# Optimization experiments

Hardware: AMD Instinct MI355X
Metric: run time of the kernel (lower is better)

Reference implementation:

```python
import jax, jax.numpy as jnp
import numpy as np

D = 1024  # in_features
H = 16    # head_num

def setup_inputs() -> dict:
    key = jax.random.key(0)
    ks = jax.random.split(key, 11)
    S, B = 2048, 2
    scale = 1.0 / np.sqrt(D)
    inp = {
        'q': jax.random.normal(ks[0], (S, B, D), jnp.float32),
        'k': jax.random.normal(ks[1], (S, B, D), jnp.float32),
        'v': jax.random.normal(ks[2], (S, B, D), jnp.float32),
        'Wq': jax.random.normal(ks[3], (D, D), jnp.float32) * scale,
        'Wk': jax.random.normal(ks[4], (D, D), jnp.float32) * scale,
        'Wv': jax.random.normal(ks[5], (D, D), jnp.float32) * scale,
        'Wo': jax.random.normal(ks[6], (D, D), jnp.float32) * scale,
        'bq': jax.random.normal(ks[7], (D,), jnp.float32) * 0.01,
        'bk': jax.random.normal(ks[8], (D,), jnp.float32) * 0.01,
        'bv': jax.random.normal(ks[9], (D,), jnp.float32) * 0.01,
        'bo': jax.random.normal(ks[10], (D,), jnp.float32) * 0.01,
    }
    return inp

def reference(q, k, v, Wq, Wk, Wv, Wo, bq, bk, bv, bo):
    # q,k,v: (S, B, D) -> (B, S, D)
    q = jnp.transpose(q, (1, 0, 2))
    k = jnp.transpose(k, (1, 0, 2))
    v = jnp.transpose(v, (1, 0, 2))
    # linear + ReLU (torch Linear: x @ W.T + b)
    qh = jax.nn.relu(q @ Wq.T + bq)
    kh = jax.nn.relu(k @ Wk.T + bk)
    vh = jax.nn.relu(v @ Wv.T + bv)
    B, S, _ = qh.shape
    hd = D // H
    # (B, S, H, hd) -> (B, H, S, hd)
    qh = qh.reshape(B, S, H, hd).transpose(0, 2, 1, 3)
    kh = kh.reshape(B, S, H, hd).transpose(0, 2, 1, 3)
    vh = vh.reshape(B, S, H, hd).transpose(0, 2, 1, 3)
    scores = jnp.einsum('bhsd,bhtd->bhst', qh, kh) / np.sqrt(hd).astype(np.float32)
    attn = jax.nn.softmax(scores, axis=-1)
    y = jnp.einsum('bhst,bhtd->bhsd', attn, vh)  # (B, H, S, hd)
    y = y.transpose(0, 2, 1, 3).reshape(B, S, D)
    y = jax.nn.relu(y @ Wo.T + bo)
    return jnp.transpose(y, (1, 0, 2))  # (S, B, D)
```

## Files before the change

### kernel.cpp

```cpp
#include <hip/hip_runtime.h>
#include <stdint.h>

typedef __attribute__((ext_vector_type(8))) short bf8v;
typedef __attribute__((ext_vector_type(4))) float f4v;
typedef __attribute__((ext_vector_type(16))) float f16v;
typedef __attribute__((ext_vector_type(4))) unsigned int u4v;

__device__ __forceinline__ unsigned short f2bf(float f) {
  unsigned int u = __float_as_uint(f);
  u += 0x7fffu + ((u >> 16) & 1u);
  return (unsigned short)(u >> 16);
}

__device__ __forceinline__ float bf2f(unsigned short s) {
  return __uint_as_float((unsigned)s << 16);
}

__device__ __forceinline__ void gload16(const void* g, void* l) {
  __builtin_amdgcn_global_load_lds(
      (__attribute__((address_space(1))) void*)reinterpret_cast<uintptr_t>(g),
      (__attribute__((address_space(3))) void*)reinterpret_cast<uintptr_t>(l),
      16, 0, 0);
}

__device__ __forceinline__ unsigned cvtpk(float lo, float hi) {
  unsigned r;
  asm("v_cvt_pk_bf16_f32 %0, %1, %2" : "=v"(r) : "v"(lo), "v"(hi));
  return r;
}

#define PAIR_SWAP(x, y) asm("v_permlane32_swap_b32 %0, %1" : "+v"(x), "+v"(y))

__global__ __launch_bounds__(256) void cvt_all(
    const float* __restrict__ s0, const float* __restrict__ s1,
    const float* __restrict__ s2, const float* __restrict__ s3,
    const float* __restrict__ s4, const float* __restrict__ s5,
    const float* __restrict__ s6, unsigned short* __restrict__ dst) {
  const size_t NA = (size_t)1 << 22, NW = (size_t)1 << 20;
  size_t i = ((size_t)blockIdx.x * 256 + threadIdx.x) * 8;
  const float* src;
  size_t off;
  if (i < 3 * NA) {
    int a = (int)(i >> 22);
    src = (a == 0) ? s0 : (a == 1) ? s1 : s2;
    off = i & (NA - 1);
  } else {
    size_t j = i - 3 * NA;
    int a = (int)(j >> 20);
    src = (a == 0) ? s3 : (a == 1) ? s4 : (a == 2) ? s5 : s6;
    off = j & (NW - 1);
  }
  const f4v* sp = (const f4v*)(src + off);
  f4v x = sp[0], y = sp[1];
  bf8v r;
  r[0] = (short)f2bf(x[0]); r[1] = (short)f2bf(x[1]);
  r[2] = (short)f2bf(x[2]); r[3] = (short)f2bf(x[3]);
  r[4] = (short)f2bf(y[0]); r[5] = (short)f2bf(y[1]);
  r[6] = (short)f2bf(y[2]); r[7] = (short)f2bf(y[3]);
  *(bf8v*)(dst + i) = r;
}

template <int OMODE, int TN>
__device__ __forceinline__ void gemm_body(
    unsigned short* Al, unsigned short* Bl,
    const unsigned short* __restrict__ A, const unsigned short* __restrict__ W,
    const float* __restrict__ bias, void* __restrict__ out) {
  const int tid = threadIdx.x;
  const int w = tid >> 6, l = tid & 63;
  const int lr = l >> 4, lc = l & 15;
  const int m0 = blockIdx.x * 128, n0 = blockIdx.y * TN;
  const int wr = w >> 1, wc = w & 1;
  const int JW = TN / 32;
  const int BCPW = TN / 64;
  const int BBUF = TN * 32;

  f4v acc[4][JW];
#pragma unroll
  for (int i = 0; i < 4; i++)
#pragma unroll
    for (int j = 0; j < JW; j++) acc[i][j] = (f4v)(0.0f);

  const int NK = 32;
#pragma unroll
  for (int i = 0; i < 2; i++) {
    int chunk = w * 2 + i;
    int e = chunk * 512 + l * 8;
    int r = e >> 5, k = e & 31;
    gload16(A + (size_t)(m0 + r) * 1024 + k, Al + chunk * 512);
  }
#pragma unroll
  for (int i = 0; i < BCPW; i++) {
    int chunk = w * BCPW + i;
    int e = chunk * 512 + l * 8;
    int r = e >> 5, k = e & 31;
    gload16(W + (size_t)(n0 + r) * 1024 + k, Bl + chunk * 512);
  }

  for (int kk = 0; kk < NK; kk++) {
    const int cur = kk & 1;
    __syncthreads();
    if (kk + 1 < NK) {
#pragma unroll
      for (int i = 0; i < 2; i++) {
        int chunk = w * 2 + i;
        int e = chunk * 512 + l * 8;
        int r = e >> 5, k = (kk + 1) * 32 + (e & 31);
        gload16(A + (size_t)(m0 + r) * 1024 + k, Al + (cur ^ 1) * 4096 + chunk * 512);
      }
#pragma unroll
      for (int i = 0; i < BCPW; i++) {
        int chunk = w * BCPW + i;
        int e = chunk * 512 + l * 8;
        int r = e >> 5, k = (kk + 1) * 32 + (e & 31);
        gload16(W + (size_t)(n0 + r) * 1024 + k, Bl + (cur ^ 1) * BBUF + chunk * 512);
      }
    }
    bf8v av[4], bv[JW];
#pragma unroll
    for (int i = 0; i < 4; i++) {
      int row = wr * 64 + i * 16 + lc;
      av[i] = *(const bf8v*)(Al + cur * 4096 + row * 32 + lr * 8);
    }
#pragma unroll
    for (int j = 0; j < JW; j++) {
      int row = wc * (TN / 2) + j * 16 + lc;
      bv[j] = *(const bf8v*)(Bl + cur * BBUF + row * 32 + lr * 8);
    }
#pragma unroll
    for (int i = 0; i < 4; i++)
#pragma unroll
      for (int j = 0; j < JW; j++)
        acc[i][j] = __builtin_amdgcn_mfma_f32_16x16x32_bf16(av[i], bv[j], acc[i][j], 0, 0, 0);
  }

#pragma unroll
  for (int j = 0; j < JW; j++) {
    int n = n0 + wc * (TN / 2) + j * 16 + lc;
    float bj = bias[n];
#pragma unroll
    for (int i = 0; i < 4; i++) {
      int mb = m0 + wr * 64 + i * 16 + lr * 4;
#pragma unroll
      for (int q = 0; q < 4; q++) {
        float val = fmaxf(acc[i][j][q] + bj, 0.0f);
        int m = mb + q;
        if (OMODE == 2) {
          int s = m & 2047, b = m >> 11;
          ((float*)out)[(size_t)(s * 2 + b) * 1024 + n] = val;
        } else {
          int s = m >> 1, b = m & 1;
          int h = n >> 6, d = n & 63;
          if (OMODE == 0)
            ((unsigned short*)out)[((size_t)(b * 16 + h) * 2048 + s) * 64 + d] = f2bf(val);
          else
            ((unsigned short*)out)[((size_t)(b * 16 + h) * 64 + d) * 2048 + s] = f2bf(val);
        }
      }
    }
  }
}

__global__ __launch_bounds__(256) void qkv_gemm(
    const unsigned short* __restrict__ qA, const unsigned short* __restrict__ kA,
    const unsigned short* __restrict__ vA,
    const unsigned short* __restrict__ Wq, const unsigned short* __restrict__ Wk,
    const unsigned short* __restrict__ Wv,
    const float* __restrict__ bq, const float* __restrict__ bk,
    const float* __restrict__ bv,
    unsigned short* __restrict__ Qh, unsigned short* __restrict__ Kh,
    unsigned short* __restrict__ Vt) {
  __shared__ __align__(16) unsigned short Al[2 * 4096];
  __shared__ __align__(16) unsigned short Bl[2 * 4096];
  int z = blockIdx.z;
  if (z == 0)      gemm_body<0, 128>(Al, Bl, qA, Wq, bq, Qh);
  else if (z == 1) gemm_body<0, 128>(Al, Bl, kA, Wk, bk, Kh);
  else             gemm_body<1, 128>(Al, Bl, vA, Wv, bv, Vt);
}

__global__ __launch_bounds__(256) void out_gemm(
    const unsigned short* __restrict__ Y, const unsigned short* __restrict__ Wo,
    const float* __restrict__ bo, float* __restrict__ out) {
  __shared__ __align__(16) unsigned short Al[2 * 4096];
  __shared__ __align__(16) unsigned short Bl[2 * 2048];
  gemm_body<2, 64>(Al, Bl, Y, Wo, bo, out);
}

__global__ __launch_bounds__(256, 2) void attn_kernel(
    const unsigned short* __restrict__ Qh, const unsigned short* __restrict__ Kh,
    const unsigned short* __restrict__ Vt,
    unsigned short* __restrict__ PO, float2* __restrict__ ML) {
  __shared__ __align__(16) unsigned short Kl[2][4096];
  __shared__ __align__(16) unsigned short Vl[2][4096];
  const int tid = threadIdx.x, w = tid >> 6, l = tid & 63;
  const int lo = l & 31, hi = l >> 5;
  const int bh = blockIdx.y;
  const int z = blockIdx.z;
  const int tbeg = z << 10, tend = tbeg + 1024;
  const int q0 = blockIdx.x * 256 + w * 64;
  const size_t qkbase = (size_t)bh * 2048 * 64;
  const size_t vtbase = (size_t)bh * 64 * 2048;
  const float cs = 0.125f * 1.44269504088896341f;

  bf8v qf[2][4];
#pragma unroll
  for (int s = 0; s < 2; s++)
#pragma unroll
    for (int c = 0; c < 4; c++)
      qf[s][c] = *(const bf8v*)(Qh + qkbase + (size_t)(q0 + s * 32 + lo) * 64 + c * 16 + hi * 8);

  f16v oacc[2][2];
  oacc[0][0] = (f16v)(0.0f); oacc[0][1] = (f16v)(0.0f);
  oacc[1][0] = (f16v)(0.0f); oacc[1][1] = (f16v)(0.0f);
  float mrun[2] = {-1e30f, -1e30f};
  float lrun[2] = {0.0f, 0.0f};

  const int swl = (lo & 7) << 4;
  int akb[4], avb[2][2][2];
#pragma unroll
  for (int c = 0; c < 4; c++) akb[c] = lo * 128 + ((c * 32 + hi * 16) ^ swl);
#pragma unroll
  for (int dt = 0; dt < 2; dt++)
#pragma unroll
    for (int kvh = 0; kvh < 2; kvh++)
#pragma unroll
      for (int kc = 0; kc < 2; kc++)
        avb[dt][kvh][kc] = (dt * 32 + lo) * 128 + ((kvh * 64 + kc * 32 + hi * 16) ^ swl);

  int stE[2], stD[2], stKV[2];
#pragma unroll
  for (int i = 0; i < 2; i++) {
    int o = (w * 2 + i) * 1024 + l * 16;
    int row = o >> 7;
    stE[i] = (o ^ ((row & 7) << 4)) >> 1;
    stD[i] = stE[i] >> 6;
    stKV[i] = stE[i] & 63;
  }
  const char* KlB = (const char*)&Kl[0][0];
  const char* VlB = (const char*)&Vl[0][0];

  auto STAGE = [&](int buf, int t0) {
#pragma unroll
    for (int i = 0; i < 2; i++) {
      gload16(Kh + qkbase + (size_t)t0 * 64 + stE[i], (char*)&Kl[buf][0] + (w * 2 + i) * 1024);
      gload16(Vt + vtbase + (size_t)stD[i] * 2048 + t0 + stKV[i], (char*)&Vl[buf][0] + (w * 2 + i) * 1024);
    }
  };

  auto COMPUTE = [&](int bo) {
#pragma unroll
    for (int kvh = 0; kvh < 2; kvh++) {
      bf8v kf[4];
#pragma unroll
      for (int c = 0; c < 4; c++)
        kf[c] = *(const bf8v*)(KlB + bo + kvh * 4096 + akb[c]);
      f16v sa = (f16v)(0.0f), sb = (f16v)(0.0f);
#pragma unroll
      for (int c = 0; c < 4; c++) {
        sa = __builtin_amdgcn_mfma_f32_32x32x16_bf16(kf[c], qf[0][c], sa, 0, 0, 0);
        sb = __builtin_amdgcn_mfma_f32_32x32x16_bf16(kf[c], qf[1][c], sb, 0, 0, 0);
      }
      bf8v vf[2][2];
#pragma unroll
      for (int dt = 0; dt < 2; dt++)
#pragma unroll
        for (int kc = 0; kc < 2; kc++)
          vf[dt][kc] = *(const bf8v*)(VlB + bo + avb[dt][kvh][kc]);

#pragma unroll
      for (int s = 0; s < 2; s++) {
        const f16v& sc16 = (s == 0) ? sa : sb;
        float t0 = fmaxf(fmaxf(sc16[0], sc16[1]), sc16[2]);
        float t1 = fmaxf(fmaxf(sc16[3], sc16[4]), sc16[5]);
        float t2 = fmaxf(fmaxf(sc16[6], sc16[7]), sc16[8]);
        float t3 = fmaxf(fmaxf(sc16[9], sc16[10]), sc16[11]);
        float t4 = fmaxf(fmaxf(sc16[12], sc16[13]), sc16[14]);
        float lm = fmaxf(fmaxf(fmaxf(t0, t1), fmaxf(t2, t3)), fmaxf(t4, sc16[15]));
        float msc = lm * cs;
        if (!__all(msc <= mrun[s] + 8.0f)) {
          float x = msc, y = msc;
          PAIR_SWAP(x, y);
          float pm = fmaxf(x, y);
          float mnew = fmaxf(mrun[s], pm);
          float scl = __builtin_amdgcn_exp2f(mrun[s] - mnew);
          lrun[s] *= scl;
#pragma unroll
          for (int dt = 0; dt < 2; dt++)
#pragma unroll
            for (int r = 0; r < 16; r++) oacc[s][dt][r] *= scl;
          mrun[s] = mnew;
        }
        float p[16];
#pragma unroll
        for (int r = 0; r < 16; r++)
          p[r] = __builtin_amdgcn_exp2f(sc16[r] * cs - mrun[s]);
        float s01 = (p[0] + p[1]) + (p[2] + p[3]);
        float s23 = (p[4] + p[5]) + (p[6] + p[7]);
        float s45 = (p[8] + p[9]) + (p[10] + p[11]);
        float s67 = (p[12] + p[13]) + (p[14] + p[15]);
        lrun[s] += (s01 + s23) + (s45 + s67);
        bf8v pf[2];
#pragma unroll
        for (int kc = 0; kc < 2; kc++) {
          unsigned a0 = cvtpk(p[kc * 8 + 0], p[kc * 8 + 1]);
          unsigned a1 = cvtpk(p[kc * 8 + 2], p[kc * 8 + 3]);
          unsigned b0 = cvtpk(p[kc * 8 + 4], p[kc * 8 + 5]);
          unsigned b1 = cvtpk(p[kc * 8 + 6], p[kc * 8 + 7]);
          PAIR_SWAP(a0, b0);
          PAIR_SWAP(a1, b1);
          u4v pw;
          pw[0] = a0; pw[1] = a1; pw[2] = b0; pw[3] = b1;
          pf[kc] = __builtin_bit_cast(bf8v, pw);
        }
#pragma unroll
        for (int dt = 0; dt < 2; dt++)
#pragma unroll
          for (int kc = 0; kc < 2; kc++)
            oacc[s][dt] = __builtin_amdgcn_mfma_f32_32x32x16_bf16(vf[dt][kc], pf[kc],
                                                                 oacc[s][dt], 0, 0, 0);
      }
    }
  };

  STAGE(0, tbeg);
  __syncthreads();
#pragma unroll 1
  for (int t0 = tbeg; t0 < tend; t0 += 128) {
    STAGE(1, t0 + 64);
    COMPUTE(0);
    __syncthreads();
    if (t0 + 128 < tend) STAGE(0, t0 + 128);
    COMPUTE(8192);
    __syncthreads();
  }

#pragma unroll
  for (int s = 0; s < 2; s++) {
    float x = lrun[s], y = lrun[s];
    PAIR_SWAP(x, y);
    float lt = x + y;
    int q = q0 + s * 32 + lo;
    size_t prow = (size_t)(z * 32 + bh) * 2048 + q;
    if (hi == 0) ML[prow] = float2{mrun[s], lt};
    unsigned short* pp = PO + prow * 64;
#pragma unroll
    for (int dt = 0; dt < 2; dt++)
#pragma unroll
      for (int r = 0; r < 16; r++) {
        int d = dt * 32 + (r & 3) + 8 * (r >> 2) + 4 * hi;
        pp[d] = f2bf(oacc[s][dt][r]);
      }
  }
}

__global__ __launch_bounds__(256) void combine_kernel(
    const unsigned short* __restrict__ PO, const float2* __restrict__ ML,
    unsigned short* __restrict__ Y) {
  int idx = blockIdx.x * 256 + threadIdx.x;
  int row = idx >> 1, hr = idx & 1;
  int bh = row >> 11, q = row & 2047;
  float2 ml0 = ML[row], ml1 = ML[65536 + row];
  float M = fmaxf(ml0.x, ml1.x);
  float a0 = __builtin_amdgcn_exp2f(ml0.x - M);
  float a1 = __builtin_amdgcn_exp2f(ml1.x - M);
  float L = ml0.y * a0 + ml1.y * a1;
  float s0 = a0 / L, s1 = a1 / L;
  const unsigned short* p0 = PO + (size_t)row * 64 + hr * 32;
  const unsigned short* p1 = PO + ((size_t)65536 + row) * 64 + hr * 32;
  int b = bh >> 4, h = bh & 15;
  unsigned short* yp = Y + (((size_t)(b * 2048 + q)) << 10) + h * 64 + hr * 32;
#pragma unroll
  for (int g = 0; g < 4; g++) {
    bf8v v0 = *(const bf8v*)(p0 + g * 8);
    bf8v v1 = *(const bf8v*)(p1 + g * 8);
    bf8v r;
#pragma unroll
    for (int j = 0; j < 8; j++)
      r[j] = (short)f2bf(bf2f((unsigned short)v0[j]) * s0 +
                         bf2f((unsigned short)v1[j]) * s1);
    *(bf8v*)(yp + g * 8) = r;
  }
}

extern "C" void kernel_launch(void* const* d_in, const int* in_sizes, int n_in,
                              void* d_out, int out_size, void* d_ws, size_t ws_size,
                              hipStream_t stream) {
  const float* q  = (const float*)d_in[0];
  const float* k  = (const float*)d_in[1];
  const float* v  = (const float*)d_in[2];
  const float* Wq = (const float*)d_in[3];
  const float* Wk = (const float*)d_in[4];
  const float* Wv = (const float*)d_in[5];
  const float* Wo = (const float*)d_in[6];
  const float* bq = (const float*)d_in[7];
  const float* bk = (const float*)d_in[8];
  const float* bv = (const float*)d_in[9];
  const float* bo = (const float*)d_in[10];

  const size_t NA = (size_t)4096 * 1024;
  const size_t NW = (size_t)1024 * 1024;
  unsigned short* qA  = (unsigned short*)d_ws;
  unsigned short* kA  = qA  + NA;
  unsigned short* vA  = kA  + NA;
  unsigned short* WqB = vA  + NA;
  unsigned short* WkB = WqB + NW;
  unsigned short* WvB = WkB + NW;
  unsigned short* WoB = WvB + NW;
  unsigned short* Qh  = WoB + NW;
  unsigned short* Kh  = Qh  + NA;
  unsigned short* Vt  = Kh  + NA;
  unsigned short* Y   = Vt  + NA;

  unsigned short* PO = qA;
  float2*         ML = (float2*)vA;

  cvt_all<<<dim3(8192), 256, 0, stream>>>(q, k, v, Wq, Wk, Wv, Wo, qA);

  qkv_gemm<<<dim3(32, 8, 3), 256, 0, stream>>>(qA, kA, vA, WqB, WkB, WvB,
                                               bq, bk, bv, Qh, Kh, Vt);
  attn_kernel<<<dim3(8, 32, 2), 256, 0, stream>>>(Qh, Kh, Vt, PO, ML);
  combine_kernel<<<dim3(512), 256, 0, stream>>>(PO, ML, Y);
  out_gemm<<<dim3(32, 16), 256, 0, stream>>>(Y, WoB, bo, (float*)d_out);
}
```

Baseline: 127.7 us.

## Split attention KV into four chunks, raise occupancy, prioritize MFMA waves

When the workspace is large enough, the attention kernel now splits the KV range four ways instead of two, doubling the grid to fill more CUs. A generalized combine kernel merges the partial outputs. The kernel's launch bound now asks for 4 blocks per SIMD, and s_setprio raises wave priority around the MFMA groups. The lazy rescale threshold also drops from 8 to 5. The split adds partial-output traffic and a heavier combine step, and the tighter launch bound may force register spills.

```diff
diff --git a/kernel.cpp b/kernel.cpp
--- a/kernel.cpp
+++ b/kernel.cpp
@@ -185,17 +185,17 @@
   gemm_body<2, 64>(Al, Bl, Y, Wo, bo, out);
 }
 
-__global__ __launch_bounds__(256, 2) void attn_kernel(
+__global__ __launch_bounds__(256, 4) void attn_kernel(
     const unsigned short* __restrict__ Qh, const unsigned short* __restrict__ Kh,
     const unsigned short* __restrict__ Vt,
-    unsigned short* __restrict__ PO, float2* __restrict__ ML) {
+    unsigned short* __restrict__ PO, float2* __restrict__ ML, int kvlen) {
   __shared__ __align__(16) unsigned short Kl[2][4096];
   __shared__ __align__(16) unsigned short Vl[2][4096];
   const int tid = threadIdx.x, w = tid >> 6, l = tid & 63;
   const int lo = l & 31, hi = l >> 5;
   const int bh = blockIdx.y;
   const int z = blockIdx.z;
-  const int tbeg = z << 10, tend = tbeg + 1024;
+  const int tbeg = z * kvlen, tend = tbeg + kvlen;
   const int q0 = blockIdx.x * 256 + w * 64;
   const size_t qkbase = (size_t)bh * 2048 * 64;
   const size_t vtbase = (size_t)bh * 64 * 2048;
@@ -254,11 +254,13 @@
       for (int c = 0; c < 4; c++)
         kf[c] = *(const bf8v*)(KlB + bo + kvh * 4096 + akb[c]);
       f16v sa = (f16v)(0.0f), sb = (f16v)(0.0f);
+      __builtin_amdgcn_s_setprio(1);
 #pragma unroll
       for (int c = 0; c < 4; c++) {
         sa = __builtin_amdgcn_mfma_f32_32x32x16_bf16(kf[c], qf[0][c], sa, 0, 0, 0);
         sb = __builtin_amdgcn_mfma_f32_32x32x16_bf16(kf[c], qf[1][c], sb, 0, 0, 0);
       }
+      __builtin_amdgcn_s_setprio(0);
       bf8v vf[2][2];
 #pragma unroll
       for (int dt = 0; dt < 2; dt++)
@@ -276,7 +278,7 @@
         float t4 = fmaxf(fmaxf(sc16[12], sc16[13]), sc16[14]);
         float lm = fmaxf(fmaxf(fmaxf(t0, t1), fmaxf(t2, t3)), fmaxf(t4, sc16[15]));
         float msc = lm * cs;
-        if (!__all(msc <= mrun[s] + 8.0f)) {
+        if (!__all(msc <= mrun[s] + 5.0f)) {
           float x = msc, y = msc;
           PAIR_SWAP(x, y);
           float pm = fmaxf(x, y);
@@ -311,12 +313,14 @@
           pw[0] = a0; pw[1] = a1; pw[2] = b0; pw[3] = b1;
           pf[kc] = __builtin_bit_cast(bf8v, pw);
         }
+        __builtin_amdgcn_s_setprio(1);
 #pragma unroll
         for (int dt = 0; dt < 2; dt++)
 #pragma unroll
           for (int kc = 0; kc < 2; kc++)
             oacc[s][dt] = __builtin_amdgcn_mfma_f32_32x32x16_bf16(vf[dt][kc], pf[kc],
                                                                  oacc[s][dt], 0, 0, 0);
+        __builtin_amdgcn_s_setprio(0);
       }
     }
   };
@@ -352,31 +356,45 @@
   }
 }
 
+template <int SPL>
 __global__ __launch_bounds__(256) void combine_kernel(
     const unsigned short* __restrict__ PO, const float2* __restrict__ ML,
     unsigned short* __restrict__ Y) {
   int idx = blockIdx.x * 256 + threadIdx.x;
   int row = idx >> 1, hr = idx & 1;
   int bh = row >> 11, q = row & 2047;
-  float2 ml0 = ML[row], ml1 = ML[65536 + row];
-  float M = fmaxf(ml0.x, ml1.x);
-  float a0 = __builtin_amdgcn_exp2f(ml0.x - M);
-  float a1 = __builtin_amdgcn_exp2f(ml1.x - M);
-  float L = ml0.y * a0 + ml1.y * a1;
-  float s0 = a0 / L, s1 = a1 / L;
-  const unsigned short* p0 = PO + (size_t)row * 64 + hr * 32;
-  const unsigned short* p1 = PO + ((size_t)65536 + row) * 64 + hr * 32;
+  float2 ml[SPL];
+  float M = -1e30f;
+#pragma unroll
+  for (int i = 0; i < SPL; i++) {
+    ml[i] = ML[i * 65536 + row];
+    M = fmaxf(M, ml[i].x);
+  }
+  float a[SPL], L = 0.0f;
+#pragma unroll
+  for (int i = 0; i < SPL; i++) {
+    a[i] = __builtin_amdgcn_exp2f(ml[i].x - M);
+    L += ml[i].y * a[i];
+  }
+  float invL = 1.0f / L;
+#pragma unroll
+  for (int i = 0; i < SPL; i++) a[i] *= invL;
   int b = bh >> 4, h = bh & 15;
   unsigned short* yp = Y + (((size_t)(b * 2048 + q)) << 10) + h * 64 + hr * 32;
 #pragma unroll
   for (int g = 0; g < 4; g++) {
-    bf8v v0 = *(const bf8v*)(p0 + g * 8);
-    bf8v v1 = *(const bf8v*)(p1 + g * 8);
+    float accv[8];
+#pragma unroll
+    for (int j = 0; j < 8; j++) accv[j] = 0.0f;
+#pragma unroll
+    for (int i = 0; i < SPL; i++) {
+      bf8v v = *(const bf8v*)(PO + ((size_t)i * 65536 + row) * 64 + hr * 32 + g * 8);
+#pragma unroll
+      for (int j = 0; j < 8; j++) accv[j] += bf2f((unsigned short)v[j]) * a[i];
+    }
     bf8v r;
 #pragma unroll
-    for (int j = 0; j < 8; j++)
-      r[j] = (short)f2bf(bf2f((unsigned short)v0[j]) * s0 +
-                         bf2f((unsigned short)v1[j]) * s1);
+    for (int j = 0; j < 8; j++) r[j] = (short)f2bf(accv[j]);
     *(bf8v*)(yp + g * 8) = r;
   }
 }
@@ -410,14 +428,28 @@
   unsigned short* Vt  = Kh  + NA;
   unsigned short* Y   = Vt  + NA;
 
-  unsigned short* PO = qA;
-  float2*         ML = (float2*)vA;
+  const size_t need4 = (size_t)(32 + 32 + 2) * 1024 * 1024 + ((size_t)4 * 65536 * 8);
+  int SPL;
+  unsigned short* PO;
+  float2* ML;
+  if (ws_size >= need4) {
+    SPL = 4;
+    PO = Y + NA;
+    ML = (float2*)(PO + 4 * NA);
+  } else {
+    SPL = 2;
+    PO = qA;
+    ML = (float2*)vA;
+  }
 
   cvt_all<<<dim3(8192), 256, 0, stream>>>(q, k, v, Wq, Wk, Wv, Wo, qA);
 
   qkv_gemm<<<dim3(32, 8, 3), 256, 0, stream>>>(qA, kA, vA, WqB, WkB, WvB,
                                                bq, bk, bv, Qh, Kh, Vt);
-  attn_kernel<<<dim3(8, 32, 2), 256, 0, stream>>>(Qh, Kh, Vt, PO, ML);
-  combine_kernel<<<dim3(512), 256, 0, stream>>>(PO, ML, Y);
+  attn_kernel<<<dim3(8, 32, SPL), 256, 0, stream>>>(Qh, Kh, Vt, PO, ML, 2048 / SPL);
+  if (SPL == 4)
+    combine_kernel<4><<<dim3(512), 256, 0, stream>>>(PO, ML, Y);
+  else
+    combine_kernel<2><<<dim3(512), 256, 0, stream>>>(PO, ML, Y);
   out_gemm<<<dim3(32, 16), 256, 0, stream>>>(Y, WoB, bo, (float*)d_out);
 }
```

New measurement: 302.6 us. +137.1%, slower.
